# Optimization experiments

Hardware: AMD Instinct MI355X
Metric: run time of the kernel (lower is better)

Reference implementation:

```python
import jax, jax.numpy as jnp
import numpy as np

B, V = 4, 10242
N = B * V            # 40968 packed vertices
E_PER = 30720        # edges per mesh
HID = 128


def _bilinear_sample(fm, grid):
    """pytorch3d vert_align core: grid_sample(align_corners=True, bilinear).
    fm: [B,C,H,W], grid: [B,V,2] xy in [-1,1] -> [B,V,C]."""
    b_, c_, h_, w_ = fm.shape
    x = (grid[..., 0] + 1.0) * 0.5 * (w_ - 1)
    y = (grid[..., 1] + 1.0) * 0.5 * (h_ - 1)
    x0f, y0f = jnp.floor(x), jnp.floor(y)
    wx1, wy1 = x - x0f, y - y0f
    wx0, wy0 = 1.0 - wx1, 1.0 - wy1
    x0 = jnp.clip(x0f, 0, w_ - 1).astype(jnp.int32)
    x1 = jnp.clip(x0f + 1, 0, w_ - 1).astype(jnp.int32)
    y0 = jnp.clip(y0f, 0, h_ - 1).astype(jnp.int32)
    y1 = jnp.clip(y0f + 1, 0, h_ - 1).astype(jnp.int32)
    fmt = jnp.transpose(fm, (0, 2, 3, 1))  # [B,H,W,C]
    bi = jnp.arange(b_)[:, None]
    g = lambda yy, xx: fmt[bi, yy, xx]     # [B,V,C]
    return ((wy0 * wx0)[..., None] * g(y0, x0)
            + (wy0 * wx1)[..., None] * g(y0, x1)
            + (wy1 * wx0)[..., None] * g(y1, x0)
            + (wy1 * wx1)[..., None] * g(y1, x1))


def _graph_conv(x, edges, w0, b0, w1, b1):
    """pytorch3d GraphConv (undirected): W0 x_i + sum over both edge dirs of W1 x_j."""
    h0 = x @ w0 + b0
    h1 = x @ w1 + b1
    e0, e1 = edges[:, 0], edges[:, 1]
    agg = jnp.zeros_like(h0).at[e0].add(h1[e1]).at[e1].add(h1[e0])
    return h0 + agg


def setup_inputs() -> dict:
    key = jax.random.key(0)
    ks = jax.random.split(key, 20)
    s = 0.05
    # per-mesh edges, offset into packed index space
    e = jax.random.randint(ks[0], (B, E_PER, 2), 0, V)
    e = e + (jnp.arange(B) * V)[:, None, None]
    return {
        "feat1": jax.random.normal(ks[1], (B, 256, 56, 56), jnp.float32),
        "feat2": jax.random.normal(ks[2], (B, 512, 28, 28), jnp.float32),
        "feat3": jax.random.normal(ks[3], (B, 1024, 14, 14), jnp.float32),
        "feat4": jax.random.normal(ks[4], (B, 2048, 7, 7), jnp.float32),
        "aligned_verts": jax.random.uniform(ks[5], (B, V, 3), jnp.float32, -1.0, 1.0),
        "verts_packed": jax.random.normal(ks[6], (N, 3), jnp.float32),
        "image_enc": jax.random.normal(ks[7], (B, 256), jnp.float32),
        "edges": e.reshape(B * E_PER, 2).astype(jnp.int64),
        "bottleneck_w": jax.random.normal(ks[8], (3840, HID), jnp.float32) * s,
        "bottleneck_b": jnp.zeros((HID,), jnp.float32),
        "g0_w0": jax.random.normal(ks[9], (387, HID), jnp.float32) * s,
        "g0_b0": jnp.zeros((HID,), jnp.float32),
        "g0_w1": jax.random.normal(ks[10], (387, HID), jnp.float32) * s,
        "g0_b1": jnp.zeros((HID,), jnp.float32),
        "gw0": jax.random.normal(ks[11], (7, HID, HID), jnp.float32) * s,
        "gb0": jnp.zeros((7, HID), jnp.float32),
        "gw1": jax.random.normal(ks[12], (7, HID, HID), jnp.float32) * s,
        "gb1": jnp.zeros((7, HID), jnp.float32),
        "off_w": jax.random.normal(ks[13], (HID, 3), jnp.float32) * s,
        "off_b": jnp.zeros((3,), jnp.float32),
    }


def reference(feat1, feat2, feat3, feat4, aligned_verts, verts_packed, image_enc,
              edges, bottleneck_w, bottleneck_b, g0_w0, g0_b0, g0_w1, g0_b1,
              gw0, gb0, gw1, gb1, off_w, off_b):
    grid = aligned_verts[..., :2]  # vert_align uses xy only
    samp = jnp.concatenate([_bilinear_sample(f, grid)
                            for f in (feat1, feat2, feat3, feat4)], axis=-1)
    samp = samp.reshape(N, 3840)  # return_packed=True
    vfeat = jax.nn.relu(samp @ bottleneck_w + bottleneck_b)
    enc = jnp.repeat(image_enc, V, axis=0)  # repeat_interleave
    x = jnp.concatenate([vfeat, verts_packed, enc], axis=1)  # [N,387]
    x = jax.nn.relu(_graph_conv(x, edges, g0_w0, g0_b0, g0_w1, g0_b1))
    for i in range(7):
        x = jax.nn.relu(_graph_conv(x, edges, gw0[i], gb0[i], gw1[i], gb1[i]))
    return x @ off_w + off_b  # delta_v [N,3]
```

## Files before the change

kernel.cpp:

```cpp
#include <hip/hip_runtime.h>

static inline int ceil_div(int a, int b) { return (a + b - 1) / b; }

typedef __attribute__((ext_vector_type(8))) short short8;
typedef __attribute__((ext_vector_type(4))) float floatx4;

__device__ __forceinline__ unsigned short f2bf(float f) {
    unsigned int u = __float_as_uint(f);
    unsigned int r = (u + 0x7fffu + ((u >> 16) & 1u)) >> 16;
    return (unsigned short)r;
}
__device__ __forceinline__ float bf2f(unsigned short h) {
    return __uint_as_float(((unsigned int)h) << 16);
}

__global__ __launch_bounds__(1024) void scan1_k(const int* __restrict__ deg,
                                                int* __restrict__ excl,
                                                int* __restrict__ bsum, int Nv) {
    __shared__ int s[1024];
    int tid = threadIdx.x;
    int i = blockIdx.x * 1024 + tid;
    int v = (i < Nv) ? deg[i] : 0;
    s[tid] = v;
    __syncthreads();
    for (int off = 1; off < 1024; off <<= 1) {
        int t = (tid >= off) ? s[tid - off] : 0;
        __syncthreads();
        if (tid >= off) s[tid] += t;
        __syncthreads();
    }
    if (i < Nv) excl[i] = s[tid] - v;
    if (tid == 1023) bsum[blockIdx.x] = s[1023];
}

__global__ __launch_bounds__(64) void scan2_k(int* __restrict__ bsum, int nb) {
    __shared__ int s[64];
    int tid = threadIdx.x;
    int v = (tid < nb) ? bsum[tid] : 0;
    s[tid] = v;
    __syncthreads();
    for (int off = 1; off < 64; off <<= 1) {
        int t = (tid >= off) ? s[tid - off] : 0;
        __syncthreads();
        if (tid >= off) s[tid] += t;
        __syncthreads();
    }
    if (tid < nb) bsum[tid] = s[tid] - v;
}

__global__ __launch_bounds__(1024) void scan3_k(const int* __restrict__ excl,
                                                const int* __restrict__ bsum,
                                                const int* __restrict__ deg,
                                                int* __restrict__ rowptr,
                                                int* __restrict__ cursor, int Nv) {
    int i = blockIdx.x * 1024 + threadIdx.x;
    if (i < Nv) {
        int val = excl[i] + bsum[blockIdx.x];
        rowptr[i] = val;
        cursor[i] = val;
        if (i == Nv - 1) rowptr[Nv] = val + deg[i];
    }
}

__global__ __launch_bounds__(256) void fill_adj_k(const int* __restrict__ edges,
                                                  int* __restrict__ cursor,
                                                  int* __restrict__ adj, int E) {
    int e = blockIdx.x * blockDim.x + threadIdx.x;
    if (e < E) {
        int a = edges[2 * e], b = edges[2 * e + 1];
        adj[atomicAdd(&cursor[a], 1)] = b;
        adj[atomicAdd(&cursor[b], 1)] = a;
    }
}

__global__ __launch_bounds__(256) void fatpre_k(const int* __restrict__ edges,
                                                int* __restrict__ deg, int E, int nE,
                                                const float* __restrict__ g0w0,
                                                const float* __restrict__ g0w1,
                                                const float* __restrict__ gw0,
                                                const float* __restrict__ gw1,
                                                unsigned short* __restrict__ Wt,
                                                const float* __restrict__ bw,
                                                unsigned short* __restrict__ bwT,
                                                const float* __restrict__ enc,
                                                float* __restrict__ encp, int B_) {
    int bid = blockIdx.x;
    int tid = threadIdx.x;
    if (bid < nE) {
        int e = bid * 256 + tid;
        if (e < E) {
            atomicAdd(&deg[edges[2 * e]], 1);
            atomicAdd(&deg[edges[2 * e + 1]], 1);
        }
    } else if (bid < nE + 16) {
        int lh = bid - nE;
        int l = lh >> 1, h = lh & 1;
        const float* src;
        if (l == 0) src = h ? g0w1 : g0w0;
        else src = (h ? gw1 : gw0) + (size_t)(l - 1) * 16384;
        unsigned short* dst = Wt + (size_t)lh * 16384;
        for (int idx = tid; idx < 16384; idx += 256) {
            int n = idx >> 7, k = idx & 127;
            dst[n * 128 + k] = f2bf(src[k * 128 + n]);
        }
    } else if (bid < nE + 46) {
        int blk = bid - nE - 16;
        for (int idx = tid; idx < 16384; idx += 256) {
            int n = idx >> 7, kk = idx & 127;
            bwT[(size_t)n * 3840 + blk * 128 + kk] =
                f2bf(bw[(size_t)(blk * 128 + kk) * 128 + n]);
        }
    } else {
        int b = bid - nE - 46;
        int sH = tid >> 7;
        int j = tid & 127;
        const float* w = sH ? g0w1 : g0w0;
        const float* eb = enc + b * 256;
        float acc = 0.f;
        for (int c = 0; c < 256; ++c) acc = fmaf(eb[c], w[(131 + c) * 128 + j], acc);
        encp[(sH * B_ + b) * 128 + j] = acc;
    }
}

__global__ __launch_bounds__(256) void proj_all_k(
    const float* __restrict__ fm1, const float* __restrict__ fm2,
    const float* __restrict__ fm3, const float* __restrict__ fm4,
    const unsigned short* __restrict__ bwT, float* __restrict__ o1, float* __restrict__ o2,
    float* __restrict__ o3, float* __restrict__ o4, int B_) {
    __shared__ unsigned short wlds[8192];

    int tid = threadIdx.x;
    int n1 = 49 * B_ * 4, n2 = 13 * B_ * 8, n3 = 4 * B_ * 16;
    int bid = blockIdx.x;
    const float* fm;
    float* op;
    int C, HW, PT, idx, koff;
    if (bid < n1) {
        fm = fm1; op = o1; C = 256; HW = 3136; PT = 49; idx = bid; koff = 0;
    } else if (bid < n1 + n2) {
        fm = fm2; op = o2; C = 512; HW = 784; PT = 13; idx = bid - n1; koff = 256;
    } else if (bid < n1 + n2 + n3) {
        fm = fm3; op = o3; C = 1024; HW = 196; PT = 4; idx = bid - n1 - n2; koff = 768;
    } else {
        fm = fm4; op = o4; C = 2048; HW = 49; PT = 1; idx = bid - n1 - n2 - n3; koff = 1792;
    }
    int pt = idx % PT;
    int r2 = idx / PT;
    int b = r2 % B_;
    int zz = r2 / B_;
    int p0 = pt * 64;
    const float* fmb = fm + (size_t)b * C * HW;
    int kcf = zz * 64;
    int kcw = koff + kcf;

#pragma unroll
    for (int l = 0; l < 4; ++l) {
        int i2 = tid + l * 256;
        int n = i2 >> 3, c16 = i2 & 7;
        *(short8*)&wlds[n * 64 + ((c16 ^ (n & 7)) * 8)] =
            *(const short8*)(bwT + (size_t)n * 3840 + kcw + c16 * 8);
    }

    int wave = tid >> 6, lane = tid & 63;
    int row16 = lane & 15, quad = lane >> 4;
    int p = p0 + wave * 16 + row16;
    bool pok = (p < HW);
    int pc = pok ? p : 0;
    short8 ax[2];
#pragma unroll
    for (int ks = 0; ks < 2; ++ks) {
#pragma unroll
        for (int j = 0; j < 8; ++j) {
            float v = pok ? fmb[(size_t)(kcf + ks * 32 + quad * 8 + j) * HW + pc] : 0.f;
            ax[ks][j] = (short)f2bf(v);
        }
    }
    __syncthreads();

    floatx4 acc[8];
#pragma unroll
    for (int j = 0; j < 8; ++j) acc[j] = (floatx4){0.f, 0.f, 0.f, 0.f};
#pragma unroll
    for (int ks = 0; ks < 2; ++ks) {
        int c = ks * 4 + quad;
#pragma unroll
        for (int nt = 0; nt < 8; ++nt) {
            int wr = nt * 16 + row16;
            short8 bwf = *(short8*)&wlds[wr * 64 + ((c ^ (wr & 7)) * 8)];
            acc[nt] = __builtin_amdgcn_mfma_f32_16x16x32_bf16(ax[ks], bwf, acc[nt], 0, 0, 0);
        }
    }

    float* obase = op + (size_t)b * HW * 128;
#pragma unroll
    for (int nt = 0; nt < 8; ++nt) {
        int colg = nt * 16 + row16;
#pragma unroll
        for (int rr = 0; rr < 4; ++rr) {
            int pr = p0 + wave * 16 + quad * 4 + rr;
            if (pr < HW) atomicAdd(&obase[(size_t)pr * 128 + colg], acc[nt][rr]);
        }
    }
}

__device__ __forceinline__ float sample_level(const float* __restrict__ pp, int Hh, int Ww,
                                              float gx, float gy, int j) {
    float x = (gx + 1.f) * 0.5f * (float)(Ww - 1);
    float y = (gy + 1.f) * 0.5f * (float)(Hh - 1);
    float x0f = floorf(x), y0f = floorf(y);
    float wx1 = x - x0f, wy1 = y - y0f;
    float wx0 = 1.f - wx1, wy0 = 1.f - wy1;
    int x0 = (int)fminf(fmaxf(x0f, 0.f), (float)(Ww - 1));
    int x1 = (int)fminf(fmaxf(x0f + 1.f, 0.f), (float)(Ww - 1));
    int y0 = (int)fminf(fmaxf(y0f, 0.f), (float)(Hh - 1));
    int y1 = (int)fminf(fmaxf(y0f + 1.f, 0.f), (float)(Hh - 1));
    const float* r00 = pp + (size_t)(y0 * Ww + x0) * 128;
    const float* r01 = pp + (size_t)(y0 * Ww + x1) * 128;
    const float* r10 = pp + (size_t)(y1 * Ww + x0) * 128;
    const float* r11 = pp + (size_t)(y1 * Ww + x1) * 128;
    return wy0 * (wx0 * r00[j] + wx1 * r01[j]) + wy1 * (wx0 * r10[j] + wx1 * r11[j]);
}

__global__ __launch_bounds__(128) void sample_bottleneck_k(
    const float* __restrict__ av, const float* __restrict__ pp1, const float* __restrict__ pp2,
    const float* __restrict__ pp3, const float* __restrict__ pp4, const float* __restrict__ bb,
    const float* __restrict__ verts, const float* __restrict__ encp,
    const float* __restrict__ g0w0, const float* __restrict__ g0w1,
    const float* __restrict__ g0b0, const float* __restrict__ g0b1,
    unsigned short* __restrict__ X, unsigned short* __restrict__ H, int V_, int B_) {
    int n = blockIdx.x, j = threadIdx.x;
    int b = n / V_;
    float gx = av[(size_t)n * 3 + 0];
    float gy = av[(size_t)n * 3 + 1];
    float acc = bb[j];
    acc += sample_level(pp1 + (size_t)b * 3136 * 128, 56, 56, gx, gy, j);
    acc += sample_level(pp2 + (size_t)b * 784 * 128, 28, 28, gx, gy, j);
    acc += sample_level(pp3 + (size_t)b * 196 * 128, 14, 14, gx, gy, j);
    acc += sample_level(pp4 + (size_t)b * 49 * 128, 7, 7, gx, gy, j);
    X[(size_t)n * 128 + j] = f2bf(fmaxf(acc, 0.f));
    float v0 = verts[n * 3 + 0], v1 = verts[n * 3 + 1], v2 = verts[n * 3 + 2];
    float h0 = encp[(0 * B_ + b) * 128 + j] + g0b0[j] + v0 * g0w0[128 * 128 + j] +
               v1 * g0w0[129 * 128 + j] + v2 * g0w0[130 * 128 + j];
    float h1 = encp[(1 * B_ + b) * 128 + j] + g0b1[j] + v0 * g0w1[128 * 128 + j] +
               v1 * g0w1[129 * 128 + j] + v2 * g0w1[130 * 128 + j];
    H[(size_t)n * 256 + j] = f2bf(h0);
    H[(size_t)n * 256 + 128 + j] = f2bf(h1);
}

__global__ __launch_bounds__(256) void agg0_k(const unsigned short* __restrict__ X,
                                              const unsigned short* __restrict__ H,
                                              const int* __restrict__ rowptr,
                                              const int* __restrict__ adj,
                                              unsigned short* __restrict__ AggX,
                                              unsigned short* __restrict__ AggH, int Nv) {
    int wave = threadIdx.x >> 6, lane = threadIdx.x & 63;
    int n0 = (blockIdx.x * 4 + wave) * 2;
    if (n0 >= Nv) return;
    const unsigned int* Xu = (const unsigned int*)X;
    int r0 = rowptr[n0], r1 = rowptr[n0 + 1], r2 = rowptr[n0 + 2];
    float a0 = 0.f, a1 = 0.f, b0 = 0.f, b1 = 0.f;
    float c0 = 0.f, c1 = 0.f, d0 = 0.f, d1 = 0.f;
    int tA = r0, tB = r1;
    while (tA < r1 || tB < r2) {
        int nbA[8], nbB[8];
        unsigned int wA[8], wB[8], hA[8], hB[8];
#pragma unroll
        for (int q = 0; q < 8; ++q) {
            int ia = tA + q; ia = (ia < r1) ? ia : (r1 - 1); ia = (ia < 0) ? 0 : ia;
            nbA[q] = adj[ia];
            int ib = tB + q; ib = (ib < r2) ? ib : (r2 - 1); ib = (ib < 0) ? 0 : ib;
            nbB[q] = adj[ib];
        }
#pragma unroll
        for (int q = 0; q < 8; ++q) {
            wA[q] = Xu[(size_t)nbA[q] * 64 + lane];
            wB[q] = Xu[(size_t)nbB[q] * 64 + lane];
            hA[q] = *(const unsigned int*)(H + (size_t)nbA[q] * 256 + 128 + 2 * lane);
            hB[q] = *(const unsigned int*)(H + (size_t)nbB[q] * 256 + 128 + 2 * lane);
        }
#pragma unroll
        for (int q = 0; q < 8; ++q) {
            if (tA + q < r1) {
                a0 += bf2f((unsigned short)(wA[q] & 0xffff));
                a1 += bf2f((unsigned short)(wA[q] >> 16));
                c0 += bf2f((unsigned short)(hA[q] & 0xffff));
                c1 += bf2f((unsigned short)(hA[q] >> 16));
            }
            if (tB + q < r2) {
                b0 += bf2f((unsigned short)(wB[q] & 0xffff));
                b1 += bf2f((unsigned short)(wB[q] >> 16));
                d0 += bf2f((unsigned short)(hB[q] & 0xffff));
                d1 += bf2f((unsigned short)(hB[q] >> 16));
            }
        }
        tA += 8;
        tB += 8;
    }
    *(unsigned int*)(AggX + (size_t)n0 * 128 + 2 * lane) =
        (unsigned int)f2bf(a0) | ((unsigned int)f2bf(a1) << 16);
    *(unsigned int*)(AggX + (size_t)(n0 + 1) * 128 + 2 * lane) =
        (unsigned int)f2bf(b0) | ((unsigned int)f2bf(b1) << 16);
    *(unsigned int*)(AggH + (size_t)n0 * 128 + 2 * lane) =
        (unsigned int)f2bf(c0) | ((unsigned int)f2bf(c1) << 16);
    *(unsigned int*)(AggH + (size_t)(n0 + 1) * 128 + 2 * lane) =
        (unsigned int)f2bf(d0) | ((unsigned int)f2bf(d1) << 16);
}

__global__ __launch_bounds__(256) void agg_x_k(const unsigned short* __restrict__ X,
                                               const int* __restrict__ rowptr,
                                               const int* __restrict__ adj,
                                               unsigned short* __restrict__ Agg, int Nv) {
    int wave = threadIdx.x >> 6, lane = threadIdx.x & 63;
    int n0 = (blockIdx.x * 4 + wave) * 2;
    if (n0 >= Nv) return;
    const unsigned int* Xu = (const unsigned int*)X;
    int r0 = rowptr[n0], r1 = rowptr[n0 + 1], r2 = rowptr[n0 + 2];
    float a0 = 0.f, a1 = 0.f, b0 = 0.f, b1 = 0.f;
    int tA = r0, tB = r1;
    while (tA < r1 || tB < r2) {
        int nbA[8], nbB[8];
        unsigned int wA[8], wB[8];
#pragma unroll
        for (int q = 0; q < 8; ++q) {
            int ia = tA + q; ia = (ia < r1) ? ia : (r1 - 1); ia = (ia < 0) ? 0 : ia;
            nbA[q] = adj[ia];
            int ib = tB + q; ib = (ib < r2) ? ib : (r2 - 1); ib = (ib < 0) ? 0 : ib;
            nbB[q] = adj[ib];
        }
#pragma unroll
        for (int q = 0; q < 8; ++q) {
            wA[q] = Xu[(size_t)nbA[q] * 64 + lane];
            wB[q] = Xu[(size_t)nbB[q] * 64 + lane];
        }
#pragma unroll
        for (int q = 0; q < 8; ++q) {
            if (tA + q < r1) {
                a0 += bf2f((unsigned short)(wA[q] & 0xffff));
                a1 += bf2f((unsigned short)(wA[q] >> 16));
            }
            if (tB + q < r2) {
                b0 += bf2f((unsigned short)(wB[q] & 0xffff));
                b1 += bf2f((unsigned short)(wB[q] >> 16));
            }
        }
        tA += 8;
        tB += 8;
    }
    unsigned int oA = (unsigned int)f2bf(a0) | ((unsigned int)f2bf(a1) << 16);
    unsigned int oB = (unsigned int)f2bf(b0) | ((unsigned int)f2bf(b1) << 16);
    *(unsigned int*)(Agg + (size_t)n0 * 128 + 2 * lane) = oA;
    *(unsigned int*)(Agg + (size_t)(n0 + 1) * 128 + 2 * lane) = oB;
}

__global__ __launch_bounds__(256, 3) void gemm_dual_k(
    const unsigned short* __restrict__ Xin, const unsigned short* __restrict__ Agg,
    const unsigned short* __restrict__ Wt,
    const float* __restrict__ b0, const float* __restrict__ b1,
    const unsigned short* __restrict__ h0b, const unsigned short* __restrict__ aggh,
    const int* __restrict__ degv, unsigned short* __restrict__ Xout, int M) {
    __shared__ unsigned short wlds[16384];
    __shared__ unsigned short cs[64 * 72];
    __shared__ float bS[128];

    int tid = threadIdx.x;
    int m0 = blockIdx.x * 128;
    int yb = blockIdx.y;

    int wave = tid >> 6, lane = tid & 63;
    int row16 = lane & 15;
    int quad = lane >> 4;
    int wrow = wave * 16;

    short8 axT[2][4], agT[2][4];
    int dgT[2][4];
    {
        int g = min(m0 + wrow + row16, M - 1);
#pragma unroll
        for (int ks = 0; ks < 4; ++ks) {
            int koff = ks * 32 + quad * 8;
            axT[0][ks] = *(const short8*)(Xin + (size_t)g * 128 + koff);
            agT[0][ks] = *(const short8*)(Agg + (size_t)g * 128 + koff);
        }
#pragma unroll
        for (int rr = 0; rr < 4; ++rr)
            dgT[0][rr] = degv[min(m0 + wrow + quad * 4 + rr, M - 1)];
    }

    if (tid < 64) {
        bS[tid] = b0 ? b0[yb * 64 + tid] : 0.f;
        bS[64 + tid] = b1 ? b1[yb * 64 + tid] : 0.f;
    }

    const unsigned short* W0h = Wt + (size_t)yb * 64 * 128;
    const unsigned short* W1h = Wt + 16384 + (size_t)yb * 64 * 128;
#pragma unroll
    for (int l = 0; l < 8; ++l) {
        int idx = tid + l * 256;
        int half = idx >> 10;
        int r = (idx >> 4) & 63;
        int c16 = idx & 15;
        int sw = (c16 ^ (r & 15)) * 8;
        const unsigned short* src = (half ? W1h : W0h) + r * 128 + c16 * 8;
        *(short8*)&wlds[half * 8192 + r * 128 + sw] = *(const short8*)src;
    }
    __syncthreads();

    {
        int g = min(m0 + 64 + wrow + row16, M - 1);
#pragma unroll
        for (int ks = 0; ks < 4; ++ks) {
            int koff = ks * 32 + quad * 8;
            axT[1][ks] = *(const short8*)(Xin + (size_t)g * 128 + koff);
            agT[1][ks] = *(const short8*)(Agg + (size_t)g * 128 + koff);
        }
#pragma unroll
        for (int rr = 0; rr < 4; ++rr)
            dgT[1][rr] = degv[min(m0 + 64 + wrow + quad * 4 + rr, M - 1)];
    }

#pragma unroll
    for (int t = 0; t < 2; ++t) {
        int mT = m0 + t * 64;
        floatx4 acc[4];
#pragma unroll
        for (int j = 0; j < 4; j++) acc[j] = (floatx4){0.f, 0.f, 0.f, 0.f};

#pragma unroll
        for (int ks = 0; ks < 4; ++ks) {
            int c = ks * 4 + quad;
#pragma unroll
            for (int nt = 0; nt < 4; ++nt) {
                int wr = nt * 16 + row16;
                short8 bw0 = *(short8*)&wlds[wr * 128 + ((c ^ row16) * 8)];
                short8 bw1 = *(short8*)&wlds[8192 + wr * 128 + ((c ^ row16) * 8)];
                acc[nt] = __builtin_amdgcn_mfma_f32_16x16x32_bf16(axT[t][ks], bw0, acc[nt], 0, 0, 0);
                acc[nt] = __builtin_amdgcn_mfma_f32_16x16x32_bf16(agT[t][ks], bw1, acc[nt], 0, 0, 0);
            }
        }

#pragma unroll
        for (int nt = 0; nt < 4; ++nt) {
            int colh = nt * 16 + row16;
            int colg = yb * 64 + colh;
            float bc0 = bS[colh];
            float bc1 = bS[64 + colh];
#pragma unroll
            for (int rr = 0; rr < 4; ++rr) {
                int row = wrow + quad * 4 + rr;
                int gm = mT + row;
                float v = acc[nt][rr] + bc0 + (float)dgT[t][rr] * bc1;
                if (h0b && gm < M)
                    v += bf2f(h0b[(size_t)gm * 256 + colg]) +
                         bf2f(aggh[(size_t)gm * 128 + colg]);
                cs[row * 72 + colh] = f2bf(fmaxf(v, 0.f));
            }
        }
        __syncthreads();

        {
            int r = tid >> 2;
            int cq = (tid & 3) * 16;
            int gm = mT + r;
            if (gm < M) {
                unsigned short* dst = Xout + (size_t)gm * 128 + yb * 64 + cq;
                *(short8*)dst = *(short8*)&cs[r * 72 + cq];
                *(short8*)(dst + 8) = *(short8*)&cs[r * 72 + cq + 8];
            }
        }
        __syncthreads();
    }
}

__global__ __launch_bounds__(256) void head_k(const unsigned short* __restrict__ X,
                                              const float* __restrict__ off_w,
                                              const float* __restrict__ off_b,
                                              float* __restrict__ out, int Nv) {
    int wave = threadIdx.x >> 6, lane = threadIdx.x & 63;
    int n = blockIdx.x * 4 + wave;
    if (n >= Nv) return;
    unsigned int u = *(const unsigned int*)(X + (size_t)n * 128 + 2 * lane);
    float x0 = bf2f((unsigned short)(u & 0xffff));
    float x1 = bf2f((unsigned short)(u >> 16));
    int c0 = 2 * lane, c1 = 2 * lane + 1;
    float p0 = x0 * off_w[c0 * 3 + 0] + x1 * off_w[c1 * 3 + 0];
    float p1 = x0 * off_w[c0 * 3 + 1] + x1 * off_w[c1 * 3 + 1];
    float p2 = x0 * off_w[c0 * 3 + 2] + x1 * off_w[c1 * 3 + 2];
#pragma unroll
    for (int m = 1; m < 64; m <<= 1) {
        p0 += __shfl_xor(p0, m);
        p1 += __shfl_xor(p1, m);
        p2 += __shfl_xor(p2, m);
    }
    if (lane == 0) {
        out[n * 3 + 0] = p0 + off_b[0];
        out[n * 3 + 1] = p1 + off_b[1];
        out[n * 3 + 2] = p2 + off_b[2];
    }
}

extern "C" void kernel_launch(void* const* d_in, const int* in_sizes, int n_in, void* d_out,
                              int out_size, void* d_ws, size_t ws_size, hipStream_t stream) {
    const float* feat1 = (const float*)d_in[0];
    const float* feat2 = (const float*)d_in[1];
    const float* feat3 = (const float*)d_in[2];
    const float* feat4 = (const float*)d_in[3];
    const float* av = (const float*)d_in[4];
    const float* verts = (const float*)d_in[5];
    const float* image_enc = (const float*)d_in[6];
    const int* edges = (const int*)d_in[7];
    const float* bw = (const float*)d_in[8];
    const float* bb = (const float*)d_in[9];
    const float* g0w0 = (const float*)d_in[10];
    const float* g0b0 = (const float*)d_in[11];
    const float* g0w1 = (const float*)d_in[12];
    const float* g0b1 = (const float*)d_in[13];
    const float* gw0 = (const float*)d_in[14];
    const float* gb0 = (const float*)d_in[15];
    const float* gw1 = (const float*)d_in[16];
    const float* gb1 = (const float*)d_in[17];
    const float* off_w = (const float*)d_in[18];
    const float* off_b = (const float*)d_in[19];

    int B_ = in_sizes[6] / 256;
    int N_ = in_sizes[5] / 3;
    int V_ = N_ / B_;
    int E_ = in_sizes[7] / 2;

    char* wsb = (char*)d_ws;
    size_t off = 0;
    auto alloc = [&](size_t bytes) -> void* {
        void* p = (void*)(wsb + off);
        off += (bytes + 255) & ~(size_t)255;
        return p;
    };
    int S1 = B_ * 3136 * 128;
    int S2 = B_ * 784 * 128;
    int S3 = B_ * 196 * 128;
    int S4 = B_ * 49 * 128;
    float* pp1 = (float*)alloc((size_t)S1 * 4);
    float* pp2 = (float*)alloc((size_t)S2 * 4);
    float* pp3 = (float*)alloc((size_t)S3 * 4);
    float* pp4 = (float*)alloc((size_t)S4 * 4);
    size_t pp_bytes = off;
    unsigned short* XA = (unsigned short*)alloc((size_t)N_ * 128 * 2);
    unsigned short* XB = (unsigned short*)alloc((size_t)N_ * 128 * 2);
    unsigned short* AggB = (unsigned short*)alloc((size_t)N_ * 128 * 2);
    unsigned short* AggH = (unsigned short*)alloc((size_t)N_ * 128 * 2);
    unsigned short* Hb = (unsigned short*)alloc((size_t)N_ * 256 * 2);
    unsigned short* Wt = (unsigned short*)alloc((size_t)8 * 2 * 128 * 128 * 2);
    unsigned short* bwT = (unsigned short*)alloc((size_t)128 * 3840 * 2);
    float* encp = (float*)alloc((size_t)2 * B_ * 128 * 4);
    int* deg = (int*)alloc((size_t)(N_ + 1) * 4);
    int* rowptr = (int*)alloc((size_t)(N_ + 1) * 4);
    int* cursor = (int*)alloc((size_t)N_ * 4);
    int* excl = (int*)alloc((size_t)N_ * 4);
    int* bsum = (int*)alloc((size_t)64 * 4);
    int* adj = (int*)alloc((size_t)2 * E_ * 4);

    hipMemsetAsync(deg, 0, (N_ + 1) * sizeof(int), stream);
    hipMemsetAsync(wsb, 0, pp_bytes, stream);

    int nE = ceil_div(E_, 256);
    fatpre_k<<<nE + 46 + B_, 256, 0, stream>>>(edges, deg, E_, nE, g0w0, g0w1, gw0, gw1, Wt,
                                               bw, bwT, image_enc, encp, B_);

    int nb = ceil_div(N_, 1024);
    scan1_k<<<nb, 1024, 0, stream>>>(deg, excl, bsum, N_);
    scan2_k<<<1, 64, 0, stream>>>(bsum, nb);
    scan3_k<<<nb, 1024, 0, stream>>>(excl, bsum, deg, rowptr, cursor, N_);
    fill_adj_k<<<ceil_div(E_, 256), 256, 0, stream>>>(edges, cursor, adj, E_);

    int nproj = 49 * B_ * 4 + 13 * B_ * 8 + 4 * B_ * 16 + 1 * B_ * 32;
    proj_all_k<<<nproj, 256, 0, stream>>>(feat1, feat2, feat3, feat4, bwT, pp1, pp2, pp3, pp4,
                                          B_);

    sample_bottleneck_k<<<N_, 128, 0, stream>>>(av, pp1, pp2, pp3, pp4, bb, verts, encp, g0w0,
                                                g0w1, g0b0, g0b1, XA, Hb, V_, B_);

    int agrid = ceil_div(N_, 8);

    dim3 ggrid(ceil_div(N_, 128), 2);
    agg0_k<<<agrid, 256, 0, stream>>>(XA, Hb, rowptr, adj, AggB, AggH, N_);
    gemm_dual_k<<<ggrid, 256, 0, stream>>>(XA, AggB, Wt, nullptr, nullptr, Hb, AggH, deg, XB,
                                           N_);
    unsigned short* Xc = XB;
    unsigned short* Xn = XA;
    for (int i = 0; i < 7; ++i) {
        agg_x_k<<<agrid, 256, 0, stream>>>(Xc, rowptr, adj, AggB, N_);
        gemm_dual_k<<<ggrid, 256, 0, stream>>>(Xc, AggB, Wt + (size_t)(i + 1) * 32768,
                                               gb0 + i * 128, gb1 + i * 128, nullptr, nullptr,
                                               deg, Xn, N_);
        unsigned short* t = Xc;
        Xc = Xn;
        Xn = t;
    }
    head_k<<<ceil_div(N_, 4), 256, 0, stream>>>(Xc, off_w, off_b, (float*)d_out, N_);
}
```

Baseline: 471.5 us.

## Rework neighbor aggregation to 4 nodes per wave with 16B loads; double proj K-chunk

The per-layer aggregation kernel now assigns four nodes to each wave, 16 lanes per node. Each lane loads 8 bf16 values per neighbor with one 16-byte vector load, and neighbor indices are broadcast by shuffle from a single coalesced adj load. This is meant to raise memory-level parallelism and cut per-load instruction overhead in the gather. Separately, the projection kernel now processes two 64-channel K chunks per block, halving the block count and the fp32 atomic adds to the output, at the cost of an extra barrier and less parallelism.

```diff
diff --git a/kernel.cpp b/kernel.cpp
--- a/kernel.cpp
+++ b/kernel.cpp
@@ -130,7 +130,7 @@
     __shared__ unsigned short wlds[8192];
 
     int tid = threadIdx.x;
-    int n1 = 49 * B_ * 4, n2 = 13 * B_ * 8, n3 = 4 * B_ * 16;
+    int n1 = 49 * B_ * 2, n2 = 13 * B_ * 4, n3 = 4 * B_ * 8;
     int bid = blockIdx.x;
     const float* fm;
     float* op;
@@ -150,44 +150,50 @@
     int zz = r2 / B_;
     int p0 = pt * 64;
     const float* fmb = fm + (size_t)b * C * HW;
-    int kcf = zz * 64;
-    int kcw = koff + kcf;
-
-#pragma unroll
-    for (int l = 0; l < 4; ++l) {
-        int i2 = tid + l * 256;
-        int n = i2 >> 3, c16 = i2 & 7;
-        *(short8*)&wlds[n * 64 + ((c16 ^ (n & 7)) * 8)] =
-            *(const short8*)(bwT + (size_t)n * 3840 + kcw + c16 * 8);
-    }
+    int kcf0 = zz * 128;
 
     int wave = tid >> 6, lane = tid & 63;
     int row16 = lane & 15, quad = lane >> 4;
     int p = p0 + wave * 16 + row16;
     bool pok = (p < HW);
     int pc = pok ? p : 0;
-    short8 ax[2];
-#pragma unroll
-    for (int ks = 0; ks < 2; ++ks) {
-#pragma unroll
-        for (int j = 0; j < 8; ++j) {
-            float v = pok ? fmb[(size_t)(kcf + ks * 32 + quad * 8 + j) * HW + pc] : 0.f;
-            ax[ks][j] = (short)f2bf(v);
-        }
-    }
-    __syncthreads();
 
     floatx4 acc[8];
 #pragma unroll
     for (int j = 0; j < 8; ++j) acc[j] = (floatx4){0.f, 0.f, 0.f, 0.f};
-#pragma unroll
-    for (int ks = 0; ks < 2; ++ks) {
-        int c = ks * 4 + quad;
-#pragma unroll
-        for (int nt = 0; nt < 8; ++nt) {
-            int wr = nt * 16 + row16;
-            short8 bwf = *(short8*)&wlds[wr * 64 + ((c ^ (wr & 7)) * 8)];
-            acc[nt] = __builtin_amdgcn_mfma_f32_16x16x32_bf16(ax[ks], bwf, acc[nt], 0, 0, 0);
+
+#pragma unroll
+    for (int zz2 = 0; zz2 < 2; ++zz2) {
+        int kcf = kcf0 + zz2 * 64;
+        int kcw = koff + kcf;
+        if (zz2) __syncthreads();
+#pragma unroll
+        for (int l = 0; l < 4; ++l) {
+            int i2 = tid + l * 256;
+            int n = i2 >> 3, c16 = i2 & 7;
+            *(short8*)&wlds[n * 64 + ((c16 ^ (n & 7)) * 8)] =
+                *(const short8*)(bwT + (size_t)n * 3840 + kcw + c16 * 8);
+        }
+        short8 ax[2];
+#pragma unroll
+        for (int ks = 0; ks < 2; ++ks) {
+#pragma unroll
+            for (int j = 0; j < 8; ++j) {
+                float v = pok ? fmb[(size_t)(kcf + ks * 32 + quad * 8 + j) * HW + pc] : 0.f;
+                ax[ks][j] = (short)f2bf(v);
+            }
+        }
+        __syncthreads();
+#pragma unroll
+        for (int ks = 0; ks < 2; ++ks) {
+            int c = ks * 4 + quad;
+#pragma unroll
+            for (int nt = 0; nt < 8; ++nt) {
+                int wr = nt * 16 + row16;
+                short8 bwf = *(short8*)&wlds[wr * 64 + ((c ^ (wr & 7)) * 8)];
+                acc[nt] =
+                    __builtin_amdgcn_mfma_f32_16x16x32_bf16(ax[ks], bwf, acc[nt], 0, 0, 0);
+            }
         }
     }
 
@@ -309,47 +315,49 @@
 __global__ __launch_bounds__(256) void agg_x_k(const unsigned short* __restrict__ X,
                                                const int* __restrict__ rowptr,
                                                const int* __restrict__ adj,
-                                               unsigned short* __restrict__ Agg, int Nv) {
+                                               unsigned short* __restrict__ Agg, int Nv,
+                                               int Etot) {
     int wave = threadIdx.x >> 6, lane = threadIdx.x & 63;
-    int n0 = (blockIdx.x * 4 + wave) * 2;
+    int n0 = (blockIdx.x * 4 + wave) * 4;
     if (n0 >= Nv) return;
-    const unsigned int* Xu = (const unsigned int*)X;
-    int r0 = rowptr[n0], r1 = rowptr[n0 + 1], r2 = rowptr[n0 + 2];
-    float a0 = 0.f, a1 = 0.f, b0 = 0.f, b1 = 0.f;
-    int tA = r0, tB = r1;
-    while (tA < r1 || tB < r2) {
-        int nbA[8], nbB[8];
-        unsigned int wA[8], wB[8];
+    int g = lane >> 4, c = lane & 15;
+    int rp = rowptr[min(n0 + (lane & 7), Nv)];
+    int sg = __shfl(rp, g);
+    int eg = __shfl(rp, g + 1);
+    int m = eg - sg;
+    m = max(m, __shfl_xor(m, 16));
+    m = max(m, __shfl_xor(m, 32));
+
+    float acc[8];
+#pragma unroll
+    for (int j = 0; j < 8; ++j) acc[j] = 0.f;
+
+    for (int it = 0; it < m; it += 8) {
+        int t = sg + it + (lane & 7);
+        int adjv = adj[min(t, Etot - 1)];
+        short8 buf[8];
 #pragma unroll
         for (int q = 0; q < 8; ++q) {
-            int ia = tA + q; ia = (ia < r1) ? ia : (r1 - 1); ia = (ia < 0) ? 0 : ia;
-            nbA[q] = adj[ia];
-            int ib = tB + q; ib = (ib < r2) ? ib : (r2 - 1); ib = (ib < 0) ? 0 : ib;
-            nbB[q] = adj[ib];
+            int nbq = __shfl(adjv, (lane & 48) + q);
+            buf[q] = *(const short8*)(X + (size_t)nbq * 128 + c * 8);
         }
 #pragma unroll
         for (int q = 0; q < 8; ++q) {
-            wA[q] = Xu[(size_t)nbA[q] * 64 + lane];
-            wB[q] = Xu[(size_t)nbB[q] * 64 + lane];
-        }
-#pragma unroll
-        for (int q = 0; q < 8; ++q) {
-            if (tA + q < r1) {
-                a0 += bf2f((unsigned short)(wA[q] & 0xffff));
-                a1 += bf2f((unsigned short)(wA[q] >> 16));
-            }
-            if (tB + q < r2) {
-                b0 += bf2f((unsigned short)(wB[q] & 0xffff));
-                b1 += bf2f((unsigned short)(wB[q] >> 16));
-            }
-        }
-        tA += 8;
-        tB += 8;
-    }
-    unsigned int oA = (unsigned int)f2bf(a0) | ((unsigned int)f2bf(a1) << 16);
-    unsigned int oB = (unsigned int)f2bf(b0) | ((unsigned int)f2bf(b1) << 16);
-    *(unsigned int*)(Agg + (size_t)n0 * 128 + 2 * lane) = oA;
-    *(unsigned int*)(Agg + (size_t)(n0 + 1) * 128 + 2 * lane) = oB;
+            bool ok = (sg + it + q < eg);
+#pragma unroll
+            for (int j = 0; j < 8; ++j) {
+                float v = bf2f((unsigned short)buf[q][j]);
+                acc[j] += ok ? v : 0.f;
+            }
+        }
+    }
+
+    if (n0 + g < Nv) {
+        short8 o;
+#pragma unroll
+        for (int j = 0; j < 8; ++j) o[j] = (short)f2bf(acc[j]);
+        *(short8*)(Agg + (size_t)(n0 + g) * 128 + c * 8) = o;
+    }
 }
 
 __global__ __launch_bounds__(256, 3) void gemm_dual_k(
@@ -570,23 +578,22 @@
     scan3_k<<<nb, 1024, 0, stream>>>(excl, bsum, deg, rowptr, cursor, N_);
     fill_adj_k<<<ceil_div(E_, 256), 256, 0, stream>>>(edges, cursor, adj, E_);
 
-    int nproj = 49 * B_ * 4 + 13 * B_ * 8 + 4 * B_ * 16 + 1 * B_ * 32;
+    int nproj = 49 * B_ * 2 + 13 * B_ * 4 + 4 * B_ * 8 + 1 * B_ * 16;
     proj_all_k<<<nproj, 256, 0, stream>>>(feat1, feat2, feat3, feat4, bwT, pp1, pp2, pp3, pp4,
                                           B_);
 
     sample_bottleneck_k<<<N_, 128, 0, stream>>>(av, pp1, pp2, pp3, pp4, bb, verts, encp, g0w0,
                                                 g0w1, g0b0, g0b1, XA, Hb, V_, B_);
 
-    int agrid = ceil_div(N_, 8);
-
     dim3 ggrid(ceil_div(N_, 128), 2);
-    agg0_k<<<agrid, 256, 0, stream>>>(XA, Hb, rowptr, adj, AggB, AggH, N_);
+    agg0_k<<<ceil_div(N_, 8), 256, 0, stream>>>(XA, Hb, rowptr, adj, AggB, AggH, N_);
     gemm_dual_k<<<ggrid, 256, 0, stream>>>(XA, AggB, Wt, nullptr, nullptr, Hb, AggH, deg, XB,
                                            N_);
     unsigned short* Xc = XB;
     unsigned short* Xn = XA;
+    int agrid4 = ceil_div(N_, 16);
     for (int i = 0; i < 7; ++i) {
-        agg_x_k<<<agrid, 256, 0, stream>>>(Xc, rowptr, adj, AggB, N_);
+        agg_x_k<<<agrid4, 256, 0, stream>>>(Xc, rowptr, adj, AggB, N_, 2 * E_);
         gemm_dual_k<<<ggrid, 256, 0, stream>>>(Xc, AggB, Wt + (size_t)(i + 1) * 32768,
                                                gb0 + i * 128, gb1 + i * 128, nullptr, nullptr,
                                                deg, Xn, N_);
```

Result: faster. 428.4 us (-9.1%).
